# Kernel optimization log

Measured on AMD Instinct MI355X. Metric: run time of the kernel, lower is better.

Reference implementation:

```python
import jax, jax.numpy as jnp
import numpy as np
from jax.scipy.linalg import expm

U_SHAPE = (4, 32, 16, 16, 16, 3, 3)   # [mu, t, x, y, z, 3, 3]
W_SHAPE = (8, 32, 16, 16, 16, 3, 3)   # [feature, t, x, y, z, 3, 3]


def setup_inputs() -> dict:
    key = jax.random.key(0)
    k = jax.random.split(key, 5)
    return {
        "U_re": jax.random.normal(k[0], U_SHAPE, jnp.float32),
        "U_im": jax.random.normal(k[1], U_SHAPE, jnp.float32),
        "W_re": jax.random.normal(k[2], W_SHAPE, jnp.float32),
        "W_im": jax.random.normal(k[3], W_SHAPE, jnp.float32),
        "ah_weights": jax.random.normal(k[4], (4, W_SHAPE[0]), jnp.float32),
    }


def reference(U_re, U_im, W_re, W_im, ah_weights):
    U = (U_re + 1j * U_im).astype(jnp.complex64)
    W = (W_re + 1j * W_im).astype(jnp.complex64)

    # anti-hermitian part: W - W^dagger
    W_adj = jnp.conj(jnp.swapaxes(W, -1, -2))
    A = W - W_adj
    # traceless projection
    tr = jnp.trace(A, axis1=-2, axis2=-1)  # [i,t,x,y,z]
    A = A - (tr / 3.0)[..., None, None] * jnp.eye(3, dtype=A.dtype)

    # exponent: (1j*w) contracted with (-1j*A) == w contracted with A
    E = jnp.einsum('ui,itxyzab->utxyzab', ah_weights.astype(A.dtype), A)

    # batched 3x3 matrix exponential over the whole lattice
    E_flat = E.reshape(-1, 3, 3)
    expE = jax.vmap(expm)(E_flat).reshape(E.shape)

    # apply to gauge links: exp(...) @ U
    return jnp.einsum('utxyzij,utxyzjk->utxyzik', expE, U)
```

## Files before the change

### kernel.cpp

```cpp
#include <hip/hip_runtime.h>
#include <math.h>

#define NSITES 131072
#define SSTR   146

struct cplx { float re, im; };

__device__ __forceinline__ cplx cadd(cplx a, cplx b) { return {a.re + b.re, a.im + b.im}; }
__device__ __forceinline__ cplx csub(cplx a, cplx b) { return {a.re - b.re, a.im - b.im}; }
__device__ __forceinline__ cplx cmul(cplx a, cplx b) {
    return { fmaf(a.re, b.re, -(a.im * b.im)), fmaf(a.re, b.im, a.im * b.re) };
}
__device__ __forceinline__ cplx cmadd(cplx a, cplx b, cplx c) {
    return { fmaf(a.re, b.re, fmaf(-a.im, b.im, c.re)),
             fmaf(a.re, b.im, fmaf( a.im, b.re, c.im)) };
}
__device__ __forceinline__ cplx cscale(cplx a, float s) { return {a.re * s, a.im * s}; }

__global__ __launch_bounds__(256, 2) void lge_exp_kernel(
    const float* __restrict__ U_re, const float* __restrict__ U_im,
    const float* __restrict__ W_re, const float* __restrict__ W_im,
    const float* __restrict__ ahw,  float* __restrict__ out,
    int ucap, int wcap, int acap, int ocap)
{
    __shared__ __align__(16) float Wl[64 * SSTR];
    const int tid   = threadIdx.x;
    const int mu    = tid >> 6;
    const int lane  = tid & 63;
    const int site0 = blockIdx.x << 6;

    for (int idx = tid; idx < 4608; idx += 256) {
        int f = idx / 576;
        int r = idx - f * 576;
        int s = r / 9;
        int m = r - s * 9;
        int g = (f * NSITES + site0) * 9 + r;
        float2 v = {0.f, 0.f};
        if (g < wcap) { v.x = W_re[g]; v.y = W_im[g]; }
        ((float2*)Wl)[s * (SSTR / 2) + f * 9 + m] = v;
    }
    __syncthreads();

    const float2* wl2 = (const float2*)Wl + lane * (SSTR / 2);
    cplx E[9];
    #pragma unroll
    for (int m = 0; m < 9; m++) E[m] = {0.f, 0.f};

    #pragma unroll
    for (int f = 0; f < 8; f++) {
        float wf = (mu * 8 + f < acap) ? ahw[mu * 8 + f] : 0.f;
        float wr[9], wi[9];
        #pragma unroll
        for (int m = 0; m < 9; m++) {
            float2 v = wl2[f * 9 + m];
            wr[m] = v.x; wi[m] = v.y;
        }
        float Ar[9], Ai[9];
        #pragma unroll
        for (int a = 0; a < 3; a++)
            #pragma unroll
            for (int b = 0; b < 3; b++) {
                int ab = 3 * a + b, ba = 3 * b + a;
                Ar[ab] = wr[ab] - wr[ba];
                Ai[ab] = wi[ab] + wi[ba];
            }
        float t3 = (Ai[0] + Ai[4] + Ai[8]) * (1.f / 3.f);
        Ai[0] -= t3; Ai[4] -= t3; Ai[8] -= t3;
        #pragma unroll
        for (int m = 0; m < 9; m++) {
            E[m].re = fmaf(wf, Ar[m], E[m].re);
            E[m].im = fmaf(wf, Ai[m], E[m].im);
        }
    }

    cplx p = {0.f, 0.f};
    #pragma unroll
    for (int a = 0; a < 3; a++)
        #pragma unroll
        for (int b = 0; b < 3; b++)
            p = cmadd(E[3 * a + b], E[3 * b + a], p);
    p = cscale(p, 0.5f);

    cplx q = csub(cmul(E[0], csub(cmul(E[4], E[8]), cmul(E[5], E[7]))),
                  cmul(E[1], csub(cmul(E[3], E[8]), cmul(E[5], E[6]))));
    q = cadd(q, cmul(E[2], csub(cmul(E[3], E[7]), cmul(E[4], E[6]))));

    float r2 = 0.f;
    #pragma unroll
    for (int m = 0; m < 9; m++) r2 = fmaf(E[m].re, E[m].re, fmaf(E[m].im, E[m].im, r2));
    float rn = sqrtf(r2);

    int sc = 0;
    if (rn > 0.5f) sc = (int)ceilf(log2f(rn * 2.0f));
    sc = min(max(sc, 0), 40);
    float inv  = exp2f(-(float)sc);
    float inv2 = inv * inv;
    cplx pX = cscale(p, inv2);
    cplx qX = cscale(q, inv2 * inv);

    cplx T0 = {1.f, 0.f}, T1 = {0.f, 0.f}, T2 = {0.f, 0.f};
    cplx S0 = {1.f, 0.f}, S1 = {0.f, 0.f}, S2 = {0.f, 0.f};
    #pragma unroll
    for (int n = 1; n <= 10; n++) {
        float rcp = 1.0f / (float)n;
        cplx nT0 = cscale(cmul(T2, qX), rcp);
        cplx nT1 = cscale(cmadd(T2, pX, T0), rcp);
        cplx nT2 = cscale(T1, rcp);
        T0 = nT0; T1 = nT1; T2 = nT2;
        S0 = cadd(S0, T0); S1 = cadd(S1, T1); S2 = cadd(S2, T2);
    }

    for (int k = 0; k < sc; k++) {
        cplx f0 = S0, f1 = S1, f2 = S2;
        cplx f12 = cmul(f1, f2);
        cplx f22 = cmul(f2, f2);
        S0 = cmadd(cscale(f12, 2.f), qX, cmul(f0, f0));
        S1 = cmadd(f22, qX, cmadd(cscale(f12, 2.f), pX, cscale(cmul(f0, f1), 2.f)));
        S2 = cmadd(f22, pX, cadd(cscale(cmul(f0, f2), 2.f), cmul(f1, f1)));
    }
    cplx g0 = S0;
    cplx g1 = cscale(S1, inv);
    cplx g2 = cscale(S2, inv2);

    const int ub = (mu * NSITES + site0 + lane) * 9;
    cplx Um[9];
    const bool uok = (ub + 9 <= ucap);
    #pragma unroll
    for (int m = 0; m < 9; m++) {
        if (uok) { Um[m].re = U_re[ub + m]; Um[m].im = U_im[ub + m]; }
        else     { Um[m].re = 0.f;          Um[m].im = 0.f; }
    }

    cplx V[9];
    #pragma unroll
    for (int a = 0; a < 3; a++)
        #pragma unroll
        for (int b = 0; b < 3; b++) {
            cplx acc = cmul(E[3 * a], Um[b]);
            acc = cmadd(E[3 * a + 1], Um[3 + b], acc);
            acc = cmadd(E[3 * a + 2], Um[6 + b], acc);
            V[3 * a + b] = acc;
        }

    if (ub + 9 <= ocap) {
        float* ob = out + ub;
        #pragma unroll
        for (int a = 0; a < 3; a++)
            #pragma unroll
            for (int b = 0; b < 3; b++) {
                cplx z = cmul(E[3 * a], V[b]);
                z = cmadd(E[3 * a + 1], V[3 + b], z);
                z = cmadd(E[3 * a + 2], V[6 + b], z);
                cplx o = cmul(g0, Um[3 * a + b]);
                o = cmadd(g1, V[3 * a + b], o);
                o = cmadd(g2, z, o);
                ob[3 * a + b] = o.re;
            }
    }
}

extern "C" void kernel_launch(void* const* d_in, const int* in_sizes, int n_in,
                              void* d_out, int out_size, void* d_ws, size_t ws_size,
                              hipStream_t stream) {
    const float* U_re = (const float*)d_in[0];
    const float* U_im = (const float*)d_in[1];
    const float* W_re = (const float*)d_in[2];
    const float* W_im = (const float*)d_in[3];
    const float* ahw  = (const float*)d_in[4];
    float* out = (float*)d_out;
    const int ucap = in_sizes[0];
    const int wcap = in_sizes[2];
    const int acap = in_sizes[4];
    const int ocap = out_size;
    lge_exp_kernel<<<dim3(NSITES / 64), dim3(256), 0, stream>>>(
        U_re, U_im, W_re, W_im, ahw, out, ucap, wcap, acap, ocap);
}
```

Before: 170.1 us.

## Compute all four link directions per thread and drop shared-memory W staging

Each thread now handles one lattice site and computes the exponentials for all four directions, reading W directly from global memory instead of staging it through shared memory. This removes the redundant per-direction recomputation of the antihermitian projection and the block barrier. In exchange it quadruples per-thread register state, cuts the thread count by four, and makes the W loads strided and uncoalesced. Bounds checks on input sizes are also removed.

Result: faster. 158.6 us (-6.7%).

```diff
diff --git a/kernel.cpp b/kernel.cpp
--- a/kernel.cpp
+++ b/kernel.cpp
@@ -2,7 +2,6 @@
 #include <math.h>
 
 #define NSITES 131072
-#define SSTR   146
 
 struct cplx { float re, im; };
 
@@ -17,44 +16,26 @@
 }
 __device__ __forceinline__ cplx cscale(cplx a, float s) { return {a.re * s, a.im * s}; }
 
-__global__ __launch_bounds__(256, 2) void lge_exp_kernel(
+__global__ __launch_bounds__(256) void lge_exp_kernel(
     const float* __restrict__ U_re, const float* __restrict__ U_im,
     const float* __restrict__ W_re, const float* __restrict__ W_im,
-    const float* __restrict__ ahw,  float* __restrict__ out,
-    int ucap, int wcap, int acap, int ocap)
+    const float* __restrict__ ahw,  float* __restrict__ out)
 {
-    __shared__ __align__(16) float Wl[64 * SSTR];
-    const int tid   = threadIdx.x;
-    const int mu    = tid >> 6;
-    const int lane  = tid & 63;
-    const int site0 = blockIdx.x << 6;
+    const int s = blockIdx.x * 256 + threadIdx.x;
 
-    for (int idx = tid; idx < 4608; idx += 256) {
-        int f = idx / 576;
-        int r = idx - f * 576;
-        int s = r / 9;
-        int m = r - s * 9;
-        int g = (f * NSITES + site0) * 9 + r;
-        float2 v = {0.f, 0.f};
-        if (g < wcap) { v.x = W_re[g]; v.y = W_im[g]; }
-        ((float2*)Wl)[s * (SSTR / 2) + f * 9 + m] = v;
-    }
-    __syncthreads();
-
-    const float2* wl2 = (const float2*)Wl + lane * (SSTR / 2);
-    cplx E[9];
+    cplx E[4][9];
     #pragma unroll
-    for (int m = 0; m < 9; m++) E[m] = {0.f, 0.f};
+    for (int mu = 0; mu < 4; mu++)
+        #pragma unroll
+        for (int m = 0; m < 9; m++) E[mu][m] = {0.f, 0.f};
 
     #pragma unroll
     for (int f = 0; f < 8; f++) {
-        float wf = (mu * 8 + f < acap) ? ahw[mu * 8 + f] : 0.f;
+        const int g = (f * NSITES + s) * 9;
         float wr[9], wi[9];
         #pragma unroll
-        for (int m = 0; m < 9; m++) {
-            float2 v = wl2[f * 9 + m];
-            wr[m] = v.x; wi[m] = v.y;
-        }
+        for (int m = 0; m < 9; m++) { wr[m] = W_re[g + m]; wi[m] = W_im[g + m]; }
+
         float Ar[9], Ai[9];
         #pragma unroll
         for (int a = 0; a < 3; a++)
@@ -66,91 +47,118 @@
             }
         float t3 = (Ai[0] + Ai[4] + Ai[8]) * (1.f / 3.f);
         Ai[0] -= t3; Ai[4] -= t3; Ai[8] -= t3;
+
         #pragma unroll
-        for (int m = 0; m < 9; m++) {
-            E[m].re = fmaf(wf, Ar[m], E[m].re);
-            E[m].im = fmaf(wf, Ai[m], E[m].im);
+        for (int mu = 0; mu < 4; mu++) {
+            float wf = ahw[mu * 8 + f];
+            #pragma unroll
+            for (int m = 0; m < 9; m++) {
+                E[mu][m].re = fmaf(wf, Ar[m], E[mu][m].re);
+                E[mu][m].im = fmaf(wf, Ai[m], E[mu][m].im);
+            }
         }
     }
 
-    cplx p = {0.f, 0.f};
+    cplx pX[4], qX[4];
+    float invv[4];
+    int   sc[4];
     #pragma unroll
-    for (int a = 0; a < 3; a++)
+    for (int mu = 0; mu < 4; mu++) {
+        cplx p = {0.f, 0.f};
         #pragma unroll
-        for (int b = 0; b < 3; b++)
-            p = cmadd(E[3 * a + b], E[3 * b + a], p);
-    p = cscale(p, 0.5f);
+        for (int a = 0; a < 3; a++)
+            #pragma unroll
+            for (int b = 0; b < 3; b++)
+                p = cmadd(E[mu][3 * a + b], E[mu][3 * b + a], p);
+        p = cscale(p, 0.5f);
 
-    cplx q = csub(cmul(E[0], csub(cmul(E[4], E[8]), cmul(E[5], E[7]))),
-                  cmul(E[1], csub(cmul(E[3], E[8]), cmul(E[5], E[6]))));
-    q = cadd(q, cmul(E[2], csub(cmul(E[3], E[7]), cmul(E[4], E[6]))));
+        cplx q = csub(cmul(E[mu][0], csub(cmul(E[mu][4], E[mu][8]), cmul(E[mu][5], E[mu][7]))),
+                      cmul(E[mu][1], csub(cmul(E[mu][3], E[mu][8]), cmul(E[mu][5], E[mu][6]))));
+        q = cadd(q, cmul(E[mu][2], csub(cmul(E[mu][3], E[mu][7]), cmul(E[mu][4], E[mu][6]))));
 
-    float r2 = 0.f;
+        float r2 = 0.f;
+        #pragma unroll
+        for (int m = 0; m < 9; m++)
+            r2 = fmaf(E[mu][m].re, E[mu][m].re, fmaf(E[mu][m].im, E[mu][m].im, r2));
+        float rn = sqrtf(r2);
+
+        int k = 0;
+        if (rn > 0.5f) k = (int)ceilf(log2f(rn * 2.0f));
+        k = min(max(k, 0), 40);
+        sc[mu] = k;
+        float inv  = exp2f(-(float)k);
+        float inv2 = inv * inv;
+        invv[mu] = inv;
+        pX[mu] = cscale(p, inv2);
+        qX[mu] = cscale(q, inv2 * inv);
+    }
+
+    cplx T0[4], T1[4], T2[4], S0[4], S1[4], S2[4];
     #pragma unroll
-    for (int m = 0; m < 9; m++) r2 = fmaf(E[m].re, E[m].re, fmaf(E[m].im, E[m].im, r2));
-    float rn = sqrtf(r2);
-
-    int sc = 0;
-    if (rn > 0.5f) sc = (int)ceilf(log2f(rn * 2.0f));
-    sc = min(max(sc, 0), 40);
-    float inv  = exp2f(-(float)sc);
-    float inv2 = inv * inv;
-    cplx pX = cscale(p, inv2);
-    cplx qX = cscale(q, inv2 * inv);
-
-    cplx T0 = {1.f, 0.f}, T1 = {0.f, 0.f}, T2 = {0.f, 0.f};
-    cplx S0 = {1.f, 0.f}, S1 = {0.f, 0.f}, S2 = {0.f, 0.f};
+    for (int mu = 0; mu < 4; mu++) {
+        T0[mu] = {1.f, 0.f}; T1[mu] = {0.f, 0.f}; T2[mu] = {0.f, 0.f};
+        S0[mu] = {1.f, 0.f}; S1[mu] = {0.f, 0.f}; S2[mu] = {0.f, 0.f};
+    }
     #pragma unroll
     for (int n = 1; n <= 10; n++) {
         float rcp = 1.0f / (float)n;
-        cplx nT0 = cscale(cmul(T2, qX), rcp);
-        cplx nT1 = cscale(cmadd(T2, pX, T0), rcp);
-        cplx nT2 = cscale(T1, rcp);
-        T0 = nT0; T1 = nT1; T2 = nT2;
-        S0 = cadd(S0, T0); S1 = cadd(S1, T1); S2 = cadd(S2, T2);
+        #pragma unroll
+        for (int mu = 0; mu < 4; mu++) {
+            cplx nT0 = cscale(cmul(T2[mu], qX[mu]), rcp);
+            cplx nT1 = cscale(cmadd(T2[mu], pX[mu], T0[mu]), rcp);
+            cplx nT2 = cscale(T1[mu], rcp);
+            T0[mu] = nT0; T1[mu] = nT1; T2[mu] = nT2;
+            S0[mu] = cadd(S0[mu], T0[mu]);
+            S1[mu] = cadd(S1[mu], T1[mu]);
+            S2[mu] = cadd(S2[mu], T2[mu]);
+        }
     }
 
-    for (int k = 0; k < sc; k++) {
-        cplx f0 = S0, f1 = S1, f2 = S2;
-        cplx f12 = cmul(f1, f2);
-        cplx f22 = cmul(f2, f2);
-        S0 = cmadd(cscale(f12, 2.f), qX, cmul(f0, f0));
-        S1 = cmadd(f22, qX, cmadd(cscale(f12, 2.f), pX, cscale(cmul(f0, f1), 2.f)));
-        S2 = cmadd(f22, pX, cadd(cscale(cmul(f0, f2), 2.f), cmul(f1, f1)));
-    }
-    cplx g0 = S0;
-    cplx g1 = cscale(S1, inv);
-    cplx g2 = cscale(S2, inv2);
-
-    const int ub = (mu * NSITES + site0 + lane) * 9;
-    cplx Um[9];
-    const bool uok = (ub + 9 <= ucap);
-    #pragma unroll
-    for (int m = 0; m < 9; m++) {
-        if (uok) { Um[m].re = U_re[ub + m]; Um[m].im = U_im[ub + m]; }
-        else     { Um[m].re = 0.f;          Um[m].im = 0.f; }
+    int scm = max(max(sc[0], sc[1]), max(sc[2], sc[3]));
+    for (int k = 0; k < scm; k++) {
+        #pragma unroll
+        for (int mu = 0; mu < 4; mu++) {
+            if (k < sc[mu]) {
+                cplx f0 = S0[mu], f1 = S1[mu], f2 = S2[mu];
+                cplx f12 = cmul(f1, f2);
+                cplx f22 = cmul(f2, f2);
+                S0[mu] = cmadd(cscale(f12, 2.f), qX[mu], cmul(f0, f0));
+                S1[mu] = cmadd(f22, qX[mu], cmadd(cscale(f12, 2.f), pX[mu], cscale(cmul(f0, f1), 2.f)));
+                S2[mu] = cmadd(f22, pX[mu], cadd(cscale(cmul(f0, f2), 2.f), cmul(f1, f1)));
+            }
+        }
     }
 
-    cplx V[9];
     #pragma unroll
-    for (int a = 0; a < 3; a++)
+    for (int mu = 0; mu < 4; mu++) {
+        cplx g0 = S0[mu];
+        cplx g1 = cscale(S1[mu], invv[mu]);
+        cplx g2 = cscale(S2[mu], invv[mu] * invv[mu]);
+
+        const int ub = (mu * NSITES + s) * 9;
+        cplx Um[9];
         #pragma unroll
-        for (int b = 0; b < 3; b++) {
-            cplx acc = cmul(E[3 * a], Um[b]);
-            acc = cmadd(E[3 * a + 1], Um[3 + b], acc);
-            acc = cmadd(E[3 * a + 2], Um[6 + b], acc);
-            V[3 * a + b] = acc;
-        }
+        for (int m = 0; m < 9; m++) { Um[m].re = U_re[ub + m]; Um[m].im = U_im[ub + m]; }
 
-    if (ub + 9 <= ocap) {
+        cplx V[9];
+        #pragma unroll
+        for (int a = 0; a < 3; a++)
+            #pragma unroll
+            for (int b = 0; b < 3; b++) {
+                cplx acc = cmul(E[mu][3 * a], Um[b]);
+                acc = cmadd(E[mu][3 * a + 1], Um[3 + b], acc);
+                acc = cmadd(E[mu][3 * a + 2], Um[6 + b], acc);
+                V[3 * a + b] = acc;
+            }
+
         float* ob = out + ub;
         #pragma unroll
         for (int a = 0; a < 3; a++)
             #pragma unroll
             for (int b = 0; b < 3; b++) {
-                cplx z = cmul(E[3 * a], V[b]);
-                z = cmadd(E[3 * a + 1], V[3 + b], z);
-                z = cmadd(E[3 * a + 2], V[6 + b], z);
+                cplx z = cmul(E[mu][3 * a], V[b]);
+                z = cmadd(E[mu][3 * a + 1], V[3 + b], z);
+                z = cmadd(E[mu][3 * a + 2], V[6 + b], z);
                 cplx o = cmul(g0, Um[3 * a + b]);
                 o = cmadd(g1, V[3 * a + b], o);
                 o = cmadd(g2, z, o);
@@ -168,10 +176,6 @@
     const float* W_im = (const float*)d_in[3];
     const float* ahw  = (const float*)d_in[4];
     float* out = (float*)d_out;
-    const int ucap = in_sizes[0];
-    const int wcap = in_sizes[2];
-    const int acap = in_sizes[4];
-    const int ocap = out_size;
-    lge_exp_kernel<<<dim3(NSITES / 64), dim3(256), 0, stream>>>(
-        U_re, U_im, W_re, W_im, ahw, out, ucap, wcap, acap, ocap);
+    lge_exp_kernel<<<dim3(NSITES / 256), dim3(256), 0, stream>>>(
+        U_re, U_im, W_re, W_im, ahw, out);
 }
```

## Drop LDS staging of W; map four mu per site with direct global loads

Applied to the files above, without the earlier changes.

Removes the shared-memory staging of W and the block-wide barrier. Each thread now handles one (site, mu) pair, with the four mu threads of a site adjacent, and loads W directly from global memory so the four threads share cache lines. U loads and output stores use 3-float vector accesses, and the bounds checks and caps are dropped. In exchange, W is read four times through cache instead of once, and U/out accesses are strided by mu across lanes, which reduces coalescing.

Result: faster. 148.9 us (-12.4%).

```diff
diff --git a/kernel.cpp b/kernel.cpp
--- a/kernel.cpp
+++ b/kernel.cpp
@@ -2,7 +2,6 @@
 #include <math.h>
 
 #define NSITES 131072
-#define SSTR   146
 
 struct cplx { float re, im; };
 
@@ -17,44 +16,38 @@
 }
 __device__ __forceinline__ cplx cscale(cplx a, float s) { return {a.re * s, a.im * s}; }
 
-__global__ __launch_bounds__(256, 2) void lge_exp_kernel(
+struct __attribute__((aligned(4))) f3 { float x, y, z; };
+__device__ __forceinline__ void ld9(const float* __restrict__ p, float* r) {
+    f3 a = *(const f3*)p, b = *(const f3*)(p + 3), c = *(const f3*)(p + 6);
+    r[0] = a.x; r[1] = a.y; r[2] = a.z;
+    r[3] = b.x; r[4] = b.y; r[5] = b.z;
+    r[6] = c.x; r[7] = c.y; r[8] = c.z;
+}
+
+__global__ __launch_bounds__(256) void lge_exp_kernel(
     const float* __restrict__ U_re, const float* __restrict__ U_im,
     const float* __restrict__ W_re, const float* __restrict__ W_im,
-    const float* __restrict__ ahw,  float* __restrict__ out,
-    int ucap, int wcap, int acap, int ocap)
+    const float* __restrict__ ahw,  float* __restrict__ out)
 {
-    __shared__ __align__(16) float Wl[64 * SSTR];
-    const int tid   = threadIdx.x;
-    const int mu    = tid >> 6;
-    const int lane  = tid & 63;
-    const int site0 = blockIdx.x << 6;
+    const int gid  = blockIdx.x * 256 + threadIdx.x;
+    const int mu   = gid & 3;
+    const int site = gid >> 2;
 
-    for (int idx = tid; idx < 4608; idx += 256) {
-        int f = idx / 576;
-        int r = idx - f * 576;
-        int s = r / 9;
-        int m = r - s * 9;
-        int g = (f * NSITES + site0) * 9 + r;
-        float2 v = {0.f, 0.f};
-        if (g < wcap) { v.x = W_re[g]; v.y = W_im[g]; }
-        ((float2*)Wl)[s * (SSTR / 2) + f * 9 + m] = v;
-    }
-    __syncthreads();
+    const float4* ahw4 = (const float4*)ahw;
+    float4 wlo = ahw4[mu * 2], whi = ahw4[mu * 2 + 1];
+    const float wfv[8] = { wlo.x, wlo.y, wlo.z, wlo.w, whi.x, whi.y, whi.z, whi.w };
 
-    const float2* wl2 = (const float2*)Wl + lane * (SSTR / 2);
     cplx E[9];
     #pragma unroll
     for (int m = 0; m < 9; m++) E[m] = {0.f, 0.f};
 
     #pragma unroll
     for (int f = 0; f < 8; f++) {
-        float wf = (mu * 8 + f < acap) ? ahw[mu * 8 + f] : 0.f;
+        const int g = (f * NSITES + site) * 9;
         float wr[9], wi[9];
-        #pragma unroll
-        for (int m = 0; m < 9; m++) {
-            float2 v = wl2[f * 9 + m];
-            wr[m] = v.x; wi[m] = v.y;
-        }
+        ld9(W_re + g, wr);
+        ld9(W_im + g, wi);
+
         float Ar[9], Ai[9];
         #pragma unroll
         for (int a = 0; a < 3; a++)
@@ -66,6 +59,8 @@
             }
         float t3 = (Ai[0] + Ai[4] + Ai[8]) * (1.f / 3.f);
         Ai[0] -= t3; Ai[4] -= t3; Ai[8] -= t3;
+
+        const float wf = wfv[f];
         #pragma unroll
         for (int m = 0; m < 9; m++) {
             E[m].re = fmaf(wf, Ar[m], E[m].re);
@@ -87,7 +82,8 @@
 
     float r2 = 0.f;
     #pragma unroll
-    for (int m = 0; m < 9; m++) r2 = fmaf(E[m].re, E[m].re, fmaf(E[m].im, E[m].im, r2));
+    for (int m = 0; m < 9; m++)
+        r2 = fmaf(E[m].re, E[m].re, fmaf(E[m].im, E[m].im, r2));
     float rn = sqrtf(r2);
 
     int sc = 0;
@@ -122,14 +118,13 @@
     cplx g1 = cscale(S1, inv);
     cplx g2 = cscale(S2, inv2);
 
-    const int ub = (mu * NSITES + site0 + lane) * 9;
+    const int ub = (mu * NSITES + site) * 9;
+    float ur[9], ui[9];
+    ld9(U_re + ub, ur);
+    ld9(U_im + ub, ui);
     cplx Um[9];
-    const bool uok = (ub + 9 <= ucap);
     #pragma unroll
-    for (int m = 0; m < 9; m++) {
-        if (uok) { Um[m].re = U_re[ub + m]; Um[m].im = U_im[ub + m]; }
-        else     { Um[m].re = 0.f;          Um[m].im = 0.f; }
-    }
+    for (int m = 0; m < 9; m++) Um[m] = { ur[m], ui[m] };
 
     cplx V[9];
     #pragma unroll
@@ -142,21 +137,24 @@
             V[3 * a + b] = acc;
         }
 
-    if (ub + 9 <= ocap) {
-        float* ob = out + ub;
+    float o[9];
+    #pragma unroll
+    for (int a = 0; a < 3; a++)
         #pragma unroll
-        for (int a = 0; a < 3; a++)
-            #pragma unroll
-            for (int b = 0; b < 3; b++) {
-                cplx z = cmul(E[3 * a], V[b]);
-                z = cmadd(E[3 * a + 1], V[3 + b], z);
-                z = cmadd(E[3 * a + 2], V[6 + b], z);
-                cplx o = cmul(g0, Um[3 * a + b]);
-                o = cmadd(g1, V[3 * a + b], o);
-                o = cmadd(g2, z, o);
-                ob[3 * a + b] = o.re;
-            }
-    }
+        for (int b = 0; b < 3; b++) {
+            cplx z = cmul(E[3 * a], V[b]);
+            z = cmadd(E[3 * a + 1], V[3 + b], z);
+            z = cmadd(E[3 * a + 2], V[6 + b], z);
+            cplx oc = cmul(g0, Um[3 * a + b]);
+            oc = cmadd(g1, V[3 * a + b], oc);
+            oc = cmadd(g2, z, oc);
+            o[3 * a + b] = oc.re;
+        }
+
+    float* ob = out + ub;
+    *(f3*)(ob)     = { o[0], o[1], o[2] };
+    *(f3*)(ob + 3) = { o[3], o[4], o[5] };
+    *(f3*)(ob + 6) = { o[6], o[7], o[8] };
 }
 
 extern "C" void kernel_launch(void* const* d_in, const int* in_sizes, int n_in,
@@ -168,10 +166,6 @@
     const float* W_im = (const float*)d_in[3];
     const float* ahw  = (const float*)d_in[4];
     float* out = (float*)d_out;
-    const int ucap = in_sizes[0];
-    const int wcap = in_sizes[2];
-    const int acap = in_sizes[4];
-    const int ocap = out_size;
-    lge_exp_kernel<<<dim3(NSITES / 64), dim3(256), 0, stream>>>(
-        U_re, U_im, W_re, W_im, ahw, out, ucap, wcap, acap, ocap);
+    lge_exp_kernel<<<dim3(4 * NSITES / 256), dim3(256), 0, stream>>>(
+        U_re, U_im, W_re, W_im, ahw, out);
 }
```
